# Kernel optimization log

Measured on AMD Instinct MI355X. Metric: run time of the kernel, lower is better.

## Reference

```python
import jax, jax.numpy as jnp
import numpy as np

B, N, M = 32, 4096, 32
IN_F, OUT_F, A = 256, 256, 8


def setup_inputs() -> dict:
    key = jax.random.key(0)
    k1, k2, k3, k4, k5 = jax.random.split(key, 5)
    fatoms = jax.random.normal(k1, (B, N, IN_F), dtype=jnp.float32)
    agraph = jax.random.randint(k2, (B, N, M), 0, N, dtype=jnp.int64)
    anchor_indices = jax.random.randint(k3, (B, A), 0, N, dtype=jnp.int64)
    # xavier-uniform-like init for W and a
    wlim = float(np.sqrt(6.0 / (IN_F + OUT_F)))
    alim = float(np.sqrt(6.0 / (2 * OUT_F + 1)))
    W = jax.random.uniform(k4, (IN_F, OUT_F), dtype=jnp.float32, minval=-wlim, maxval=wlim)
    a = jax.random.uniform(k5, (2 * OUT_F, 1), dtype=jnp.float32, minval=-alim, maxval=alim)
    return {"fatoms": fatoms, "agraph": agraph, "anchor_indices": anchor_indices, "W": W, "a": a}


def reference(fatoms, agraph, anchor_indices, W, a):
    # h: (B, N, F)
    h = jnp.matmul(fatoms, W)
    F_ = h.shape[-1]
    # gather anchor features: (B, A, F)
    anchor_feat = jnp.take_along_axis(h, anchor_indices[:, :, None], axis=1)
    # e = cat([h_self + h_anch, h_self - h_anch]) @ a, decomposed to avoid the
    # (B, N, A, 2F) intermediate: e = h @ (a1+a2) + h_anch @ (a1-a2)
    a1 = a[:F_, 0]
    a2 = a[F_:, 0]
    e = (h @ (a1 + a2))[:, :, None] + (anchor_feat @ (a1 - a2))[:, None, :]  # (B, N, A)
    # mask[b,n,k] = anchor_indices[b,k] in agraph[b,n,:]  (vectorized torch.isin)
    mask = (agraph[:, :, None, :] == anchor_indices[:, None, :, None]).any(axis=-1)  # (B, N, A)
    e = jnp.where(mask, e, jnp.float32(-1e9))
    attn = jax.nn.softmax(e, axis=-1)
    # weighted sum of anchor features: (B, N, F)
    return jnp.einsum('bna,baf->bnf', attn, anchor_feat)
```

## Files before the change

kernel.cpp:

```cpp
#include <hip/hip_runtime.h>

#define B_ 32
#define N_ 4096
#define M_ 32
#define F_ 256
#define A_ 8

typedef float f32x4 __attribute__((ext_vector_type(4)));
typedef int   i32x4 __attribute__((ext_vector_type(4)));

#define WS_AF 0
#define WS_E2 (B_ * A_ * F_)
#define WS_FLAGS_F (WS_E2 + B_ * A_)

#define MASK_BLOCKS (B_ * N_ / 256)

__global__ __launch_bounds__(256) void prep_kernel(const float* __restrict__ fatoms,
                                                   const int* __restrict__ agraph,
                                                   const int* __restrict__ anchor_idx,
                                                   const float* __restrict__ W,
                                                   const float* __restrict__ a,
                                                   float* __restrict__ ws,
                                                   unsigned char* __restrict__ flags) {
    int tid = threadIdx.x;

    if (blockIdx.x < (unsigned)(B_ * A_)) {
        int bk = blockIdx.x;
        int b  = bk / A_;
        __shared__ float xs[F_];
        __shared__ float red[F_];
        int idx = anchor_idx[bk];
        xs[tid] = fatoms[((size_t)b * N_ + idx) * F_ + tid];
        __syncthreads();
        float acc[4] = {0.f, 0.f, 0.f, 0.f};
        for (int i0 = 0; i0 < F_; i0 += 16) {
#pragma unroll
            for (int j = 0; j < 16; ++j)
                acc[j & 3] += xs[i0 + j] * W[(i0 + j) * F_ + tid];
        }
        float accs = (acc[0] + acc[1]) + (acc[2] + acc[3]);
        ws[WS_AF + bk * F_ + tid] = accs;
        red[tid] = accs * (a[tid] - a[tid + F_]);
        __syncthreads();
        for (int s = 128; s > 0; s >>= 1) {
            if (tid < s) red[tid] += red[tid + s];
            __syncthreads();
        }
        if (tid == 0) ws[WS_E2 + bk] = red[0];
    } else {
        int mb   = blockIdx.x - B_ * A_;
        int b    = mb >> 4;
        int gidx = mb * 256 + tid;

        int anch[A_];
#pragma unroll
        for (int k = 0; k < A_; ++k) anch[k] = anchor_idx[b * A_ + k];

        const i32x4* gp = (const i32x4*)(agraph + (size_t)gidx * M_);
        i32x4 g[M_ / 4];
#pragma unroll
        for (int j = 0; j < M_ / 4; ++j) g[j] = gp[j];

        unsigned mk = 0;
#pragma unroll
        for (int j = 0; j < M_ / 4; ++j) {
#pragma unroll
            for (int k = 0; k < A_; ++k) {
                int hit = (g[j].x == anch[k]) | (g[j].y == anch[k]) |
                          (g[j].z == anch[k]) | (g[j].w == anch[k]);
                mk |= hit ? (1u << k) : 0u;
            }
        }
        flags[gidx] = (unsigned char)mk;
    }
}

__global__ __launch_bounds__(256) void stream_kernel(const float* __restrict__ ws,
                                                     const unsigned char* __restrict__ flags,
                                                     float* __restrict__ out) {
    int tid  = threadIdx.x;
    int w    = __builtin_amdgcn_readfirstlane(tid >> 6);
    int lane = tid & 63;
    int b    = blockIdx.x >> 4;
    int row0 = ((int)(blockIdx.x & 15) * 4 + w) * 64;

    const float* af = ws + WS_AF + b * (A_ * F_);
    f32x4 afr[A_];
#pragma unroll
    for (int k = 0; k < A_; ++k) afr[k] = *(const f32x4*)(af + k * F_ + lane * 4);

    float e2r[A_];
#pragma unroll
    for (int k = 0; k < A_; ++k) e2r[k] = ws[WS_E2 + b * A_ + k];
    float m8 = e2r[0];
#pragma unroll
    for (int k = 1; k < A_; ++k) m8 = fmaxf(m8, e2r[k]);
    float E[A_];
#pragma unroll
    for (int k = 0; k < A_; ++k) E[k] = __expf(e2r[k] - m8);

    f32x4 afm = ((afr[0] + afr[1]) + (afr[2] + afr[3])) +
                ((afr[4] + afr[5]) + (afr[6] + afr[7]));
    afm *= 0.125f;

    const unsigned* fb = (const unsigned*)(flags + (size_t)b * N_ + row0);
    unsigned f16[16];
#pragma unroll
    for (int j = 0; j < 16; ++j) f16[j] = fb[j];

    size_t base = ((size_t)b * N_ + row0) * F_ + lane * 4;
    for (int r0 = 0; r0 < 64; r0 += 4) {
        unsigned f4 = f16[r0 >> 2];
        f32x4 o[4];
        if (f4 == 0) {
#pragma unroll
            for (int u = 0; u < 4; ++u) o[u] = afm;
        } else {
#pragma unroll
            for (int u = 0; u < 4; ++u) {
                unsigned mku = (f4 >> (8 * u)) & 0xffu;
                if (mku) {
                    float p[A_], s = 0.f;
#pragma unroll
                    for (int k = 0; k < A_; ++k) {
                        p[k] = (mku & (1u << k)) ? E[k] : 0.f;
                        s += p[k];
                    }
                    float rinv = __builtin_amdgcn_rcpf(s);
                    f32x4 t = (p[0] * rinv) * afr[0];
                    t += (p[1] * rinv) * afr[1];
                    t += (p[2] * rinv) * afr[2];
                    t += (p[3] * rinv) * afr[3];
                    t += (p[4] * rinv) * afr[4];
                    t += (p[5] * rinv) * afr[5];
                    t += (p[6] * rinv) * afr[6];
                    t += (p[7] * rinv) * afr[7];
                    o[u] = t;
                } else {
                    o[u] = afm;
                }
            }
        }
#pragma unroll
        for (int u = 0; u < 4; ++u)
            *(f32x4*)(out + base + (size_t)(r0 + u) * F_) = o[u];
    }
}

extern "C" void kernel_launch(void* const* d_in, const int* in_sizes, int n_in,
                              void* d_out, int out_size, void* d_ws, size_t ws_size,
                              hipStream_t stream) {
    const float* fatoms     = (const float*)d_in[0];
    const int*   agraph     = (const int*)d_in[1];
    const int*   anchor_idx = (const int*)d_in[2];
    const float* W          = (const float*)d_in[3];
    const float* a          = (const float*)d_in[4];
    float*       out        = (float*)d_out;
    float*       ws         = (float*)d_ws;
    unsigned char* flags    = (unsigned char*)(ws + WS_FLAGS_F);

    hipLaunchKernelGGL(prep_kernel, dim3(B_ * A_ + MASK_BLOCKS), dim3(256), 0, stream,
                       fatoms, agraph, anchor_idx, W, a, ws, flags);
    hipLaunchKernelGGL(stream_kernel, dim3(B_ * (N_ / 256)), dim3(256), 0, stream,
                       ws, flags, out);
}
```

Measured before the change: 35.50 us.

## Split anchor projection into K-partials and move anchor logit reduction to stream kernel

The anchor-feature matmul is split over four K-chunks, each handled by its own block writing a partial sum to workspace. This shortens each anchor block's serial loop from 256 to 64 steps, so the prep kernel's longest block finishes sooner. The stream kernel now sums the four partials and computes the anchor logit with a wavefront shuffle reduction, which removes the LDS tree reduction and its many barriers from the prep kernel. In exchange every stream block does extra global reads and shuffle work, redundantly per wave.

```diff
diff --git a/kernel.cpp b/kernel.cpp
--- a/kernel.cpp
+++ b/kernel.cpp
@@ -9,46 +9,39 @@
 typedef float f32x4 __attribute__((ext_vector_type(4)));
 typedef int   i32x4 __attribute__((ext_vector_type(4)));
 
-#define WS_AF 0
-#define WS_E2 (B_ * A_ * F_)
-#define WS_FLAGS_F (WS_E2 + B_ * A_)
+#define WS_PART 0
+#define WS_FLAGS_F (4 * B_ * A_ * F_)
 
+#define ANCHOR_BLOCKS (4 * B_ * A_)
 #define MASK_BLOCKS (B_ * N_ / 256)
 
 __global__ __launch_bounds__(256) void prep_kernel(const float* __restrict__ fatoms,
                                                    const int* __restrict__ agraph,
                                                    const int* __restrict__ anchor_idx,
                                                    const float* __restrict__ W,
-                                                   const float* __restrict__ a,
                                                    float* __restrict__ ws,
                                                    unsigned char* __restrict__ flags) {
     int tid = threadIdx.x;
 
-    if (blockIdx.x < (unsigned)(B_ * A_)) {
-        int bk = blockIdx.x;
-        int b  = bk / A_;
-        __shared__ float xs[F_];
-        __shared__ float red[F_];
+    if (blockIdx.x < (unsigned)ANCHOR_BLOCKS) {
+        int pk = blockIdx.x & 3;
+        int bk = blockIdx.x >> 2;
+        int b  = bk >> 3;
+        __shared__ float xs[64];
         int idx = anchor_idx[bk];
-        xs[tid] = fatoms[((size_t)b * N_ + idx) * F_ + tid];
+        if (tid < 64) xs[tid] = fatoms[((size_t)b * N_ + idx) * F_ + pk * 64 + tid];
         __syncthreads();
         float acc[4] = {0.f, 0.f, 0.f, 0.f};
-        for (int i0 = 0; i0 < F_; i0 += 16) {
+        const float* wbase = W + (size_t)(pk * 64) * F_ + tid;
+        for (int i0 = 0; i0 < 64; i0 += 16) {
 #pragma unroll
             for (int j = 0; j < 16; ++j)
-                acc[j & 3] += xs[i0 + j] * W[(i0 + j) * F_ + tid];
+                acc[j & 3] += xs[i0 + j] * wbase[(size_t)(i0 + j) * F_];
         }
-        float accs = (acc[0] + acc[1]) + (acc[2] + acc[3]);
-        ws[WS_AF + bk * F_ + tid] = accs;
-        red[tid] = accs * (a[tid] - a[tid + F_]);
-        __syncthreads();
-        for (int s = 128; s > 0; s >>= 1) {
-            if (tid < s) red[tid] += red[tid + s];
-            __syncthreads();
-        }
-        if (tid == 0) ws[WS_E2 + bk] = red[0];
+        ws[WS_PART + ((size_t)pk * B_ * A_ + bk) * F_ + tid] =
+            (acc[0] + acc[1]) + (acc[2] + acc[3]);
     } else {
-        int mb   = blockIdx.x - B_ * A_;
+        int mb   = blockIdx.x - ANCHOR_BLOCKS;
         int b    = mb >> 4;
         int gidx = mb * 256 + tid;
 
@@ -77,6 +70,7 @@
 
 __global__ __launch_bounds__(256) void stream_kernel(const float* __restrict__ ws,
                                                      const unsigned char* __restrict__ flags,
+                                                     const float* __restrict__ a,
                                                      float* __restrict__ out) {
     int tid  = threadIdx.x;
     int w    = __builtin_amdgcn_readfirstlane(tid >> 6);
@@ -84,14 +78,27 @@
     int b    = blockIdx.x >> 4;
     int row0 = ((int)(blockIdx.x & 15) * 4 + w) * 64;
 
-    const float* af = ws + WS_AF + b * (A_ * F_);
     f32x4 afr[A_];
 #pragma unroll
-    for (int k = 0; k < A_; ++k) afr[k] = *(const f32x4*)(af + k * F_ + lane * 4);
+    for (int k = 0; k < A_; ++k) {
+        const float* p0 = ws + WS_PART + (size_t)(b * A_ + k) * F_ + lane * 4;
+        f32x4 t = *(const f32x4*)p0;
+        t += *(const f32x4*)(p0 + (size_t)1 * B_ * A_ * F_);
+        t += *(const f32x4*)(p0 + (size_t)2 * B_ * A_ * F_);
+        t += *(const f32x4*)(p0 + (size_t)3 * B_ * A_ * F_);
+        afr[k] = t;
+    }
 
+    f32x4 dd = *(const f32x4*)(a + lane * 4) - *(const f32x4*)(a + F_ + lane * 4);
     float e2r[A_];
 #pragma unroll
-    for (int k = 0; k < A_; ++k) e2r[k] = ws[WS_E2 + b * A_ + k];
+    for (int k = 0; k < A_; ++k) {
+        float part = afr[k].x * dd.x + afr[k].y * dd.y +
+                     afr[k].z * dd.z + afr[k].w * dd.w;
+#pragma unroll
+        for (int off = 32; off > 0; off >>= 1) part += __shfl_xor(part, off);
+        e2r[k] = part;
+    }
     float m8 = e2r[0];
 #pragma unroll
     for (int k = 1; k < A_; ++k) m8 = fmaxf(m8, e2r[k]);
@@ -159,8 +166,8 @@
     float*       ws         = (float*)d_ws;
     unsigned char* flags    = (unsigned char*)(ws + WS_FLAGS_F);
 
-    hipLaunchKernelGGL(prep_kernel, dim3(B_ * A_ + MASK_BLOCKS), dim3(256), 0, stream,
-                       fatoms, agraph, anchor_idx, W, a, ws, flags);
+    hipLaunchKernelGGL(prep_kernel, dim3(ANCHOR_BLOCKS + MASK_BLOCKS), dim3(256), 0,
+                       stream, fatoms, agraph, anchor_idx, W, ws, flags);
     hipLaunchKernelGGL(stream_kernel, dim3(B_ * (N_ / 256)), dim3(256), 0, stream,
-                       ws, flags, out);
+                       ws, flags, a, out);
 }
```

New measurement: 36.42 us. +2.6%, slower.
